# Kernel optimization log

Hardware: AMD Instinct MI355X
Metric: run time of the kernel (lower is better)

Reference implementation:

```python
import jax, jax.numpy as jnp
import numpy as np
import math

N = 50000
E = 1_600_000
F_IN = 512
F_OUT = 256
TAO = 3.0


def setup_inputs() -> dict:
    key = jax.random.key(0)
    ks = jax.random.split(key, 12)
    stdv = 1.0 / math.sqrt(F_OUT)
    std_att = 1.0 / math.sqrt(F_OUT)
    std_att_vec = 1.0 / math.sqrt(3)
    inp = {
        "inputx": jax.random.normal(ks[0], (N, F_IN), dtype=jnp.float32),
        "adj_row": jax.random.randint(ks[1], (E,), 0, N, dtype=jnp.int32),
        "adj_col": jax.random.randint(ks[2], (E,), 0, N, dtype=jnp.int32),
        "adj_val": jax.random.uniform(ks[3], (E,), dtype=jnp.float32),
        "sadj_row": jax.random.randint(ks[4], (E,), 0, N, dtype=jnp.int32),
        "sadj_col": jax.random.randint(ks[5], (E,), 0, N, dtype=jnp.int32),
        "sadj_val": jax.random.uniform(ks[6], (E,), dtype=jnp.float32),
        "weight_mlp": jax.random.uniform(ks[7], (F_IN, F_OUT), minval=-stdv, maxval=stdv, dtype=jnp.float32),
        "weight_A": jax.random.uniform(ks[8], (F_IN, F_OUT), minval=-stdv, maxval=stdv, dtype=jnp.float32),
        "weight_As": jax.random.uniform(ks[9], (F_IN, F_OUT), minval=-stdv, maxval=stdv, dtype=jnp.float32),
        "att_vec_k": jax.random.uniform(ks[10], (F_OUT, F_OUT), minval=-std_att, maxval=std_att, dtype=jnp.float32),
        "att_vec_v": jax.random.uniform(ks[11], (3, 3), minval=-std_att_vec, maxval=std_att_vec, dtype=jnp.float32),
    }
    return inp


def _spmm(row, col, val, h):
    # sparse [N,N] @ dense [N,F]: gather source rows, scale, scatter-add to dest
    msgs = val[:, None] * h[col]  # [E, F]
    return jax.ops.segment_sum(msgs, row, num_segments=N)


def reference(inputx, adj_row, adj_col, adj_val, sadj_row, sadj_col, sadj_val,
              weight_mlp, weight_A, weight_As, att_vec_k, att_vec_v):
    output_mlp = jax.nn.relu(inputx @ weight_mlp)                     # [N, F]
    output_A = jax.nn.relu(_spmm(adj_row, adj_col, adj_val, inputx @ weight_A))
    output_As = jax.nn.relu(_spmm(sadj_row, sadj_col, sadj_val, inputx @ weight_As))

    output_stru = output_mlp + output_As + output_A
    K = jnp.mean(output_stru @ att_vec_k, axis=0, keepdims=True)      # [1, F]
    logits = jnp.concatenate([output_mlp @ K.T, output_A @ K.T, output_As @ K.T], axis=1)  # [N, 3]
    att = jax.nn.softmax((jax.nn.sigmoid(logits) @ att_vec_v) / TAO, axis=1)
    alpha_mlp, alpha_A, alpha_As = att[:, 0:1], att[:, 1:2], att[:, 2:3]
    emb = alpha_mlp * output_mlp + alpha_A * output_A + alpha_As * output_As
    return emb
```

## Files before the change

### kernel.cpp

```cpp
#include <hip/hip_runtime.h>
#include <hip/hip_bf16.h>

#define N_NODES 50000
#define E_EDGES 1600000
#define FIN 512
#define FOUT 256
#define NCOMB 768
#define TAO_F 3.0f
#define M_PAD 50048
#define NB 196
#define CSTRIDE 16
#define CH 4096
#define NCH 13

#define GEMM_WGS 2346
#define GEMM_Q  (GEMM_WGS / 8)
#define GEMM_R  (GEMM_WGS % 8)

typedef __bf16 bf16x8 __attribute__((ext_vector_type(8)));
typedef float  f32x4  __attribute__((ext_vector_type(4)));

static __device__ __forceinline__ unsigned short f2bf(float f) {
    unsigned int u = __float_as_uint(f);
    u += 0x7FFFu + ((u >> 16) & 1u);
    return (unsigned short)(u >> 16);
}
static __device__ __forceinline__ float bf2f(unsigned short h) {
    return __uint_as_float(((unsigned int)h) << 16);
}

__global__ void convert_x_kernel(const float* __restrict__ X, unsigned short* __restrict__ Xb) {
    long long i = ((long long)blockIdx.x * blockDim.x + threadIdx.x) * 4;
    const long long total = (long long)M_PAD * FIN;
    if (i >= total) return;
    const long long valid = (long long)N_NODES * FIN;
    ushort4 o;
    if (i < valid) {
        const float4 v = *reinterpret_cast<const float4*>(X + i);
        o.x = f2bf(v.x); o.y = f2bf(v.y); o.z = f2bf(v.z); o.w = f2bf(v.w);
    } else {
        o.x = o.y = o.z = o.w = 0;
    }
    *reinterpret_cast<ushort4*>(Xb + i) = o;
}

__global__ void convert_w_kernel(const float* __restrict__ Wm, const float* __restrict__ Wa,
                                 const float* __restrict__ Was, unsigned short* __restrict__ Wt) {
    int i = blockIdx.x * blockDim.x + threadIdx.x;
    if (i >= NCOMB * FIN) return;
    int row = i / FIN, k = i % FIN;
    int w = row >> 8, n = row & 255;
    const float* W = (w == 0) ? Wm : (w == 1) ? Wa : Was;
    Wt[i] = f2bf(W[(size_t)k * FOUT + n]);
}

#define BM 128
#define BN 128
#define BK 64

__global__ __launch_bounds__(256) void gemm_kernel(const unsigned short* __restrict__ A,
                                                   const unsigned short* __restrict__ Bt,
                                                   float* __restrict__ Omlp,
                                                   unsigned short* __restrict__ HA,
                                                   unsigned short* __restrict__ HAs) {
    __shared__ unsigned short As[BM * BK];
    __shared__ unsigned short Bs[BN * BK];
    const int b = blockIdx.x;
    const int xcd = b & 7, ii = b >> 3;
    const int work = (xcd < GEMM_R ? xcd * (GEMM_Q + 1)
                                   : GEMM_R * (GEMM_Q + 1) + (xcd - GEMM_R) * GEMM_Q) + ii;
    const int py = work / 6, px = work - py * 6;
    const int row0 = py * BM, col0 = px * BN;
    const int tid = threadIdx.x;
    const int lane = tid & 63, wave = tid >> 6;
    const int wr = wave >> 1, wc = wave & 1;
    const int st_row = tid >> 3;
    const int st_col = (tid & 7) * 8;
    const int lds_off = wave * 512;
    const unsigned short* Ag = A + (size_t)(row0 + st_row) * FIN + st_col;
    const unsigned short* Bg = Bt + (size_t)(col0 + st_row) * FIN + st_col;
    f32x4 acc[4][4] = {};

    for (int k0 = 0; k0 < FIN; k0 += BK) {
#pragma unroll
        for (int i = 0; i < 4; i++) {
            __builtin_amdgcn_global_load_lds(
                (const __attribute__((address_space(1))) unsigned int*)(Ag + (size_t)i * 32 * FIN + k0),
                (__attribute__((address_space(3))) unsigned int*)&As[i * 2048 + lds_off], 16, 0, 0);
            __builtin_amdgcn_global_load_lds(
                (const __attribute__((address_space(1))) unsigned int*)(Bg + (size_t)i * 32 * FIN + k0),
                (__attribute__((address_space(3))) unsigned int*)&Bs[i * 2048 + lds_off], 16, 0, 0);
        }
        __syncthreads();
#pragma unroll
        for (int kk = 0; kk < 2; kk++) {
            bf16x8 af[4], bfr[4];
            const int ko = kk * 32 + (lane >> 4) * 8;
#pragma unroll
            for (int m = 0; m < 4; m++)
                af[m] = *reinterpret_cast<const bf16x8*>(&As[(wr * 64 + m * 16 + (lane & 15)) * BK + ko]);
#pragma unroll
            for (int n = 0; n < 4; n++)
                bfr[n] = *reinterpret_cast<const bf16x8*>(&Bs[(wc * 64 + n * 16 + (lane & 15)) * BK + ko]);
#pragma unroll
            for (int m = 0; m < 4; m++)
#pragma unroll
                for (int n = 0; n < 4; n++)
                    acc[m][n] = __builtin_amdgcn_mfma_f32_16x16x32_bf16(af[m], bfr[n], acc[m][n], 0, 0, 0);
        }
        __syncthreads();
    }

    const int seg = col0 >> 8;
    unsigned short* hp = (seg == 1) ? HA : HAs;
    const int rb = row0 + wr * 64 + ((lane >> 4) << 2);
    const int cb = col0 + wc * 64 + (lane & 15) - seg * 256;
#pragma unroll
    for (int m = 0; m < 4; m++)
#pragma unroll
        for (int n = 0; n < 4; n++)
#pragma unroll
            for (int j = 0; j < 4; j++) {
                int r = rb + m * 16 + j;
                if (r < N_NODES) {
                    float v = acc[m][n][j];
                    int c = cb + n * 16;
                    if (seg == 0) Omlp[(size_t)r * FOUT + c] = fmaxf(v, 0.f);
                    else          hp[(size_t)r * FOUT + c] = f2bf(v);
                }
            }
}

__global__ __launch_bounds__(256) void hist_kernel(const int* __restrict__ rowA, int* __restrict__ bcntA,
                                                   const int* __restrict__ rowS, int* __restrict__ bcntS) {
    __shared__ int h[2 * NB];
    const int t = threadIdx.x;
    for (int j = t; j < 2 * NB; j += 256) h[j] = 0;
    __syncthreads();
    int i = blockIdx.x * blockDim.x + t;
    const int stride = gridDim.x * blockDim.x;
    for (; i < E_EDGES; i += stride) {
        atomicAdd(&h[rowA[i] >> 8], 1);
        atomicAdd(&h[NB + (rowS[i] >> 8)], 1);
    }
    __syncthreads();
    for (int j = t; j < 2 * NB; j += 256) {
        int v = h[j];
        if (v) {
            if (j < NB) atomicAdd(&bcntA[j * CSTRIDE], v);
            else        atomicAdd(&bcntS[(j - NB) * CSTRIDE], v);
        }
    }
}

__global__ __launch_bounds__(256) void scan196_kernel(const int* __restrict__ bcntA, int* __restrict__ bstartA,
                                                      int* __restrict__ bcurA,
                                                      const int* __restrict__ bcntS, int* __restrict__ bstartS,
                                                      int* __restrict__ bcurS) {
    __shared__ int wsum[4];
    const int t = threadIdx.x, lane = t & 63, w = t >> 6;
    for (int g = 0; g < 2; g++) {
        const int* bcnt = g ? bcntS : bcntA;
        int* bstart = g ? bstartS : bstartA;
        int* bcur = g ? bcurS : bcurA;
        int v = (t < NB) ? bcnt[t * CSTRIDE] : 0;
        int x = v;
#pragma unroll
        for (int off = 1; off < 64; off <<= 1) { int y = __shfl_up(x, off); if (lane >= off) x += y; }
        if (lane == 63) wsum[w] = x;
        __syncthreads();
        int woff = 0;
        for (int i = 0; i < w; i++) woff += wsum[i];
        int ex = woff + x - v;
        if (t < NB) { bstart[t] = ex; bcur[t * CSTRIDE] = ex; }
        if (t == 0) bstart[NB] = E_EDGES;
        __syncthreads();
    }
}

__global__ __launch_bounds__(256) void pass1_kernel(
    const int* __restrict__ rowA, const int* __restrict__ colA, const float* __restrict__ valA,
    int* __restrict__ bcurA, int2* __restrict__ ed1A,
    const int* __restrict__ rowS, const int* __restrict__ colS, const float* __restrict__ valS,
    int* __restrict__ bcurS, int2* __restrict__ ed1S) {
    __shared__ int lcnt[NB];
    __shared__ int gcur[NB];
    const int t = threadIdx.x;
    const int base = blockIdx.x * CH;
    const int n = min(CH, E_EDGES - base);
    for (int g = 0; g < 2; g++) {
        const int* row = g ? rowS : rowA;
        const int* col = g ? colS : colA;
        const float* val = g ? valS : valA;
        int* bcur = g ? bcurS : bcurA;
        int2* ed1 = g ? ed1S : ed1A;
        for (int j = t; j < NB; j += 256) lcnt[j] = 0;
        __syncthreads();
        for (int j = t; j < n; j += 256) atomicAdd(&lcnt[row[base + j] >> 8], 1);
        __syncthreads();
        for (int j = t; j < NB; j += 256) {
            int c = lcnt[j];
            gcur[j] = c ? atomicAdd(&bcur[j * CSTRIDE], c) : 0;
        }
        __syncthreads();
        for (int j = t; j < n; j += 256) {
            int r = row[base + j];
            int b = r >> 8;
            int pos = atomicAdd(&gcur[b], 1);
            ed1[pos] = make_int2(((r & 255) << 16) | col[base + j], __float_as_int(val[base + j]));
        }
        __syncthreads();
    }
}

__global__ __launch_bounds__(256) void pass2_kernel(
    const int* __restrict__ bstartA, const int2* __restrict__ ed1A, int2* __restrict__ ed2A, int* __restrict__ rpA,
    const int* __restrict__ bstartS, const int2* __restrict__ ed1S, int2* __restrict__ ed2S, int* __restrict__ rpS) {
    const int g = (blockIdx.x >= NB) ? 1 : 0;
    const int b = blockIdx.x - g * NB;
    const int* bstart = g ? bstartS : bstartA;
    const int2* ed1 = g ? ed1S : ed1A;
    int2* ed2 = g ? ed2S : ed2A;
    int* rp = g ? rpS : rpA;
    const int s = bstart[b], e = bstart[b + 1];
    const int t = threadIdx.x, lane = t & 63, w = t >> 6;
    __shared__ int rcnt[256 * NCH];
    __shared__ int lcur[256 * NCH];
    __shared__ int wsum[4];
    for (int j = t; j < 256 * NCH; j += 256) rcnt[j] = 0;
    __syncthreads();
    for (int j = s + t; j < e; j += 256) {
        int2 v2 = ed1[j];
        atomicAdd(&rcnt[(v2.x >> 16) * NCH + ((v2.x & 0xFFFF) >> 12)], 1);
    }
    __syncthreads();
    int rsum = 0;
#pragma unroll
    for (int c = 0; c < NCH; c++) rsum += rcnt[t * NCH + c];
    int x = rsum;
#pragma unroll
    for (int off = 1; off < 64; off <<= 1) { int y = __shfl_up(x, off); if (lane >= off) x += y; }
    if (lane == 63) wsum[w] = x;
    __syncthreads();
    int woff = 0;
    for (int i = 0; i < w; i++) woff += wsum[i];
    const int ex = woff + x - rsum;
    const int row = b * 256 + t;
    if (row < N_NODES) rp[row] = s + ex;
    if (b == NB - 1 && t == 0) rp[N_NODES] = E_EDGES;
    int off2 = ex;
#pragma unroll
    for (int c = 0; c < NCH; c++) { lcur[t * NCH + c] = off2; off2 += rcnt[t * NCH + c]; }
    __syncthreads();
    for (int j = s + t; j < e; j += 256) {
        int2 v2 = ed1[j];
        int rl = v2.x >> 16, cc = (v2.x & 0xFFFF) >> 12;
        int k = atomicAdd(&lcur[rl * NCH + cc], 1);
        ed2[s + k] = make_int2(v2.x & 0xFFFF, v2.y);
    }
}

__global__ __launch_bounds__(256) void spmm_kernel(
    const int* __restrict__ rpA, const int2* __restrict__ edA,
    const unsigned short* __restrict__ HA, unsigned short* __restrict__ OA,
    const int* __restrict__ rpS, const int2* __restrict__ edS,
    const unsigned short* __restrict__ HS, unsigned short* __restrict__ OS) {
    const int gw = blockIdx.x * 4 + (threadIdx.x >> 6);
    const int lane = threadIdx.x & 63;
    const int* rp; const int2* ed; const unsigned short* H; unsigned short* O; int r;
    if (gw < N_NODES) { rp = rpA; ed = edA; H = HA; O = OA; r = gw; }
    else              { rp = rpS; ed = edS; H = HS; O = OS; r = gw - N_NODES; }
    const int s = rp[r], e = rp[r + 1];
    float a0 = 0.f, a1 = 0.f, a2 = 0.f, a3 = 0.f;
#pragma unroll 4
    for (int i = s; i < e; ++i) {
        const int2 ev = ed[i];
        const float v = __int_as_float(ev.y);
        const uint2 hv = *reinterpret_cast<const uint2*>(H + (((size_t)ev.x) << 8) + lane * 4);
        a0 += v * bf2f((unsigned short)(hv.x & 0xFFFFu));
        a1 += v * bf2f((unsigned short)(hv.x >> 16));
        a2 += v * bf2f((unsigned short)(hv.y & 0xFFFFu));
        a3 += v * bf2f((unsigned short)(hv.y >> 16));
    }
    ushort4 o;
    o.x = f2bf(fmaxf(a0, 0.f));
    o.y = f2bf(fmaxf(a1, 0.f));
    o.z = f2bf(fmaxf(a2, 0.f));
    o.w = f2bf(fmaxf(a3, 0.f));
    *reinterpret_cast<ushort4*>(O + (((size_t)r) << 8) + lane * 4) = o;
}

__global__ void colsum_kernel(const float* __restrict__ Om, const unsigned short* __restrict__ Oa,
                              const unsigned short* __restrict__ Oas, float* __restrict__ colsum) {
    const int t = threadIdx.x;
    float acc = 0.f;
    for (int r = blockIdx.x; r < N_NODES; r += gridDim.x) {
        size_t o = (size_t)r * FOUT + t;
        acc += Om[o] + bf2f(Oa[o]) + bf2f(Oas[o]);
    }
    atomicAdd(&colsum[t], acc);
}

__global__ void kvec_kernel(const float* __restrict__ colsum, const float* __restrict__ attk,
                            float* __restrict__ Kv) {
    __shared__ float mean_s[FOUT];
    const int t = threadIdx.x;
    mean_s[t] = colsum[t] * (1.0f / (float)N_NODES);
    __syncthreads();
    float acc = 0.f;
    for (int i = 0; i < FOUT; i++) acc += mean_s[i] * attk[(size_t)i * FOUT + t];
    Kv[t] = acc;
}

__global__ __launch_bounds__(256) void final_kernel(float* __restrict__ OmOut, const unsigned short* __restrict__ Oa,
                                                    const unsigned short* __restrict__ Oas, const float* __restrict__ Kv,
                                                    const float* __restrict__ attv) {
    const int r = blockIdx.x, t = threadIdx.x, lane = t & 63, w = t >> 6;
    __shared__ float red[4][3];
    __shared__ float alpha[3];
    const size_t o = (size_t)r * FOUT + t;
    const float om = OmOut[o], oa = bf2f(Oa[o]), oas = bf2f(Oas[o]);
    const float kv = Kv[t];
    float p0 = om * kv, p1 = oa * kv, p2 = oas * kv;
#pragma unroll
    for (int off = 32; off; off >>= 1) {
        p0 += __shfl_down(p0, off);
        p1 += __shfl_down(p1, off);
        p2 += __shfl_down(p2, off);
    }
    if (lane == 0) { red[w][0] = p0; red[w][1] = p1; red[w][2] = p2; }
    __syncthreads();
    if (t == 0) {
        float l0 = red[0][0] + red[1][0] + red[2][0] + red[3][0];
        float l1 = red[0][1] + red[1][1] + red[2][1] + red[3][1];
        float l2 = red[0][2] + red[1][2] + red[2][2] + red[3][2];
        float s0 = 1.f / (1.f + __expf(-l0));
        float s1 = 1.f / (1.f + __expf(-l1));
        float s2 = 1.f / (1.f + __expf(-l2));
        float q0 = (s0 * attv[0] + s1 * attv[3] + s2 * attv[6]) * (1.f / TAO_F);
        float q1 = (s0 * attv[1] + s1 * attv[4] + s2 * attv[7]) * (1.f / TAO_F);
        float q2 = (s0 * attv[2] + s1 * attv[5] + s2 * attv[8]) * (1.f / TAO_F);
        float mx = fmaxf(q0, fmaxf(q1, q2));
        float e0 = __expf(q0 - mx), e1 = __expf(q1 - mx), e2 = __expf(q2 - mx);
        float inv = 1.f / (e0 + e1 + e2);
        alpha[0] = e0 * inv; alpha[1] = e1 * inv; alpha[2] = e2 * inv;
    }
    __syncthreads();
    OmOut[o] = alpha[0] * om + alpha[1] * oa + alpha[2] * oas;
}

extern "C" void kernel_launch(void* const* d_in, const int* in_sizes, int n_in,
                              void* d_out, int out_size, void* d_ws, size_t ws_size,
                              hipStream_t stream) {
    (void)in_sizes; (void)n_in; (void)out_size; (void)ws_size;
    const float* X        = (const float*)d_in[0];
    const int*   adj_row  = (const int*)d_in[1];
    const int*   adj_col  = (const int*)d_in[2];
    const float* adj_val  = (const float*)d_in[3];
    const int*   sadj_row = (const int*)d_in[4];
    const int*   sadj_col = (const int*)d_in[5];
    const float* sadj_val = (const float*)d_in[6];
    const float* W_mlp    = (const float*)d_in[7];
    const float* W_A      = (const float*)d_in[8];
    const float* W_As     = (const float*)d_in[9];
    const float* attk     = (const float*)d_in[10];
    const float* attv     = (const float*)d_in[11];
    float* out = (float*)d_out;

    char* p = (char*)d_ws;
    auto alloc = [&](size_t bytes) -> char* {
        char* q = p; p += (bytes + 255) & ~(size_t)255; return q;
    };
    unsigned short* Xb   = (unsigned short*)alloc((size_t)M_PAD * FIN * 2);
    unsigned short* Wt   = (unsigned short*)alloc((size_t)NCOMB * FIN * 2);
    unsigned short* H_A  = (unsigned short*)alloc((size_t)N_NODES * FOUT * 2);
    unsigned short* H_As = (unsigned short*)alloc((size_t)N_NODES * FOUT * 2);
    unsigned short* O_A  = (unsigned short*)alloc((size_t)N_NODES * FOUT * 2);
    unsigned short* O_As = (unsigned short*)alloc((size_t)N_NODES * FOUT * 2);
    int2*  ed1A  = (int2*)alloc((size_t)E_EDGES * 8);
    int2*  ed1S  = (int2*)alloc((size_t)E_EDGES * 8);
    int2*  ed2A  = (int2*)alloc((size_t)E_EDGES * 8);
    int2*  ed2S  = (int2*)alloc((size_t)E_EDGES * 8);
    int*   bcntA = (int*)alloc((size_t)NB * CSTRIDE * 4);
    int*   bcntS = (int*)alloc((size_t)NB * CSTRIDE * 4);
    int*   bcurA = (int*)alloc((size_t)NB * CSTRIDE * 4);
    int*   bcurS = (int*)alloc((size_t)NB * CSTRIDE * 4);
    int*   bstartA = (int*)alloc((size_t)(NB + 1) * 4);
    int*   bstartS = (int*)alloc((size_t)(NB + 1) * 4);
    int*   rpA   = (int*)alloc((size_t)(N_NODES + 1) * 4);
    int*   rpS   = (int*)alloc((size_t)(N_NODES + 1) * 4);
    float* colsum = (float*)alloc(FOUT * 4);
    float* Kv     = (float*)alloc(FOUT * 4);

    hipMemsetAsync(bcntA, 0, (size_t)NB * CSTRIDE * 4, stream);
    hipMemsetAsync(bcntS, 0, (size_t)NB * CSTRIDE * 4, stream);
    hipMemsetAsync(colsum, 0, FOUT * 4, stream);

    {
        long long total = (long long)M_PAD * FIN / 4;
        int blocks = (int)((total + 255) / 256);
        convert_x_kernel<<<blocks, 256, 0, stream>>>(X, Xb);
    }
    convert_w_kernel<<<(NCOMB * FIN + 255) / 256, 256, 0, stream>>>(W_mlp, W_A, W_As, Wt);

    hist_kernel<<<512, 256, 0, stream>>>(adj_row, bcntA, sadj_row, bcntS);
    scan196_kernel<<<1, 256, 0, stream>>>(bcntA, bstartA, bcurA, bcntS, bstartS, bcurS);
    pass1_kernel<<<(E_EDGES + CH - 1) / CH, 256, 0, stream>>>(
        adj_row, adj_col, adj_val, bcurA, ed1A,
        sadj_row, sadj_col, sadj_val, bcurS, ed1S);
    pass2_kernel<<<2 * NB, 256, 0, stream>>>(bstartA, ed1A, ed2A, rpA,
                                             bstartS, ed1S, ed2S, rpS);

    gemm_kernel<<<GEMM_WGS, 256, 0, stream>>>(Xb, Wt, out, H_A, H_As);

    spmm_kernel<<<(2 * N_NODES) / 4, 256, 0, stream>>>(rpA, ed2A, H_A, O_A, rpS, ed2S, H_As, O_As);

    colsum_kernel<<<512, 256, 0, stream>>>(out, O_A, O_As, colsum);
    kvec_kernel<<<1, 256, 0, stream>>>(colsum, attk, Kv);
    final_kernel<<<N_NODES, 256, 0, stream>>>(out, O_A, O_As, Kv, attv);
}
```

Measured before the change: 566.2 us.

## Fuse column-sum into GEMM and SpMM epilogues, store MLP output as bf16

Removes the separate colsum kernel. Column sums are now accumulated in the GEMM epilogue for the MLP branch and in the SpMM kernel for the two graph branches, using LDS atomics followed by global atomics spread over 8 XCD-striped copies. The MLP output is stored as bf16 in a workspace buffer instead of fp32 in the output, which cuts write and read traffic. The SpMM now processes 8 consecutive rows per wave, with padded row pointers so the tail needs no bounds check. Trade-offs are bf16 rounding of the MLP branch, extra atomic traffic, and coarser SpMM load balance.

```diff
diff --git a/kernel.cpp b/kernel.cpp
--- a/kernel.cpp
+++ b/kernel.cpp
@@ -8,10 +8,13 @@
 #define NCOMB 768
 #define TAO_F 3.0f
 #define M_PAD 50048
+#define N_RPAD 50048
 #define NB 196
 #define CSTRIDE 16
 #define CH 4096
 #define NCH 13
+#define RPW 8
+#define WPG 6256
 
 #define GEMM_WGS 2346
 #define GEMM_Q  (GEMM_WGS / 8)
@@ -60,11 +63,13 @@
 
 __global__ __launch_bounds__(256) void gemm_kernel(const unsigned short* __restrict__ A,
                                                    const unsigned short* __restrict__ Bt,
-                                                   float* __restrict__ Omlp,
+                                                   unsigned short* __restrict__ Hm,
                                                    unsigned short* __restrict__ HA,
-                                                   unsigned short* __restrict__ HAs) {
+                                                   unsigned short* __restrict__ HAs,
+                                                   float* __restrict__ colsum8) {
     __shared__ unsigned short As[BM * BK];
     __shared__ unsigned short Bs[BN * BK];
+    __shared__ float csm[128];
     const int b = blockIdx.x;
     const int xcd = b & 7, ii = b >> 3;
     const int work = (xcd < GEMM_R ? xcd * (GEMM_Q + 1)
@@ -74,6 +79,7 @@
     const int tid = threadIdx.x;
     const int lane = tid & 63, wave = tid >> 6;
     const int wr = wave >> 1, wc = wave & 1;
+    if (tid < 128) csm[tid] = 0.f;
     const int st_row = tid >> 3;
     const int st_col = (tid & 7) * 8;
     const int lds_off = wave * 512;
@@ -112,9 +118,11 @@
     }
 
     const int seg = col0 >> 8;
-    unsigned short* hp = (seg == 1) ? HA : HAs;
+    unsigned short* hp = (seg == 0) ? Hm : (seg == 1) ? HA : HAs;
     const int rb = row0 + wr * 64 + ((lane >> 4) << 2);
-    const int cb = col0 + wc * 64 + (lane & 15) - seg * 256;
+    const int cb_loc = wc * 64 + (lane & 15);
+    const int cbase = col0 - seg * 256 + cb_loc;
+    float part[4] = {0.f, 0.f, 0.f, 0.f};
 #pragma unroll
     for (int m = 0; m < 4; m++)
 #pragma unroll
@@ -124,11 +132,16 @@
                 int r = rb + m * 16 + j;
                 if (r < N_NODES) {
                     float v = acc[m][n][j];
-                    int c = cb + n * 16;
-                    if (seg == 0) Omlp[(size_t)r * FOUT + c] = fmaxf(v, 0.f);
-                    else          hp[(size_t)r * FOUT + c] = f2bf(v);
+                    if (seg == 0) { v = fmaxf(v, 0.f); part[n] += v; }
+                    hp[(size_t)r * FOUT + cbase + n * 16] = f2bf(v);
                 }
             }
+    if (seg == 0) {
+#pragma unroll
+        for (int n = 0; n < 4; n++) atomicAdd(&csm[cb_loc + n * 16], part[n]);
+        __syncthreads();
+        if (tid < 128) atomicAdd(&colsum8[((b & 7) << 8) + col0 + tid], csm[tid]);
+    }
 }
 
 __global__ __launch_bounds__(256) void hist_kernel(const int* __restrict__ rowA, int* __restrict__ bcntA,
@@ -247,7 +260,7 @@
     const int ex = woff + x - rsum;
     const int row = b * 256 + t;
     if (row < N_NODES) rp[row] = s + ex;
-    if (b == NB - 1 && t == 0) rp[N_NODES] = E_EDGES;
+    else if (row <= N_RPAD) rp[row] = E_EDGES;
     int off2 = ex;
 #pragma unroll
     for (int c = 0; c < NCH; c++) { lcur[t * NCH + c] = off2; off2 += rcnt[t * NCH + c]; }
@@ -264,62 +277,80 @@
     const int* __restrict__ rpA, const int2* __restrict__ edA,
     const unsigned short* __restrict__ HA, unsigned short* __restrict__ OA,
     const int* __restrict__ rpS, const int2* __restrict__ edS,
-    const unsigned short* __restrict__ HS, unsigned short* __restrict__ OS) {
-    const int gw = blockIdx.x * 4 + (threadIdx.x >> 6);
-    const int lane = threadIdx.x & 63;
-    const int* rp; const int2* ed; const unsigned short* H; unsigned short* O; int r;
-    if (gw < N_NODES) { rp = rpA; ed = edA; H = HA; O = OA; r = gw; }
-    else              { rp = rpS; ed = edS; H = HS; O = OS; r = gw - N_NODES; }
-    const int s = rp[r], e = rp[r + 1];
-    float a0 = 0.f, a1 = 0.f, a2 = 0.f, a3 = 0.f;
+    const unsigned short* __restrict__ HS, unsigned short* __restrict__ OS,
+    float* __restrict__ colsum8) {
+    __shared__ float csum[256];
+    const int t = threadIdx.x, wave = t >> 6, lane = t & 63;
+    csum[t] = 0.f;
+    __syncthreads();
+    const int gwave = blockIdx.x * 4 + wave;
+    const int g = (gwave >= WPG) ? 1 : 0;
+    const int wv = gwave - g * WPG;
+    const int* rp = g ? rpS : rpA;
+    const int2* ed = g ? edS : edA;
+    const unsigned short* H = g ? HS : HA;
+    unsigned short* O = g ? OS : OA;
+    const int r0 = wv * RPW;
+    float cs0 = 0.f, cs1 = 0.f, cs2 = 0.f, cs3 = 0.f;
+    int s = rp[r0];
+#pragma unroll
+    for (int i = 0; i < RPW; i++) {
+        const int r = r0 + i;
+        const int e = rp[r + 1];
+        float a0 = 0.f, a1 = 0.f, a2 = 0.f, a3 = 0.f;
 #pragma unroll 4
-    for (int i = s; i < e; ++i) {
-        const int2 ev = ed[i];
-        const float v = __int_as_float(ev.y);
-        const uint2 hv = *reinterpret_cast<const uint2*>(H + (((size_t)ev.x) << 8) + lane * 4);
-        a0 += v * bf2f((unsigned short)(hv.x & 0xFFFFu));
-        a1 += v * bf2f((unsigned short)(hv.x >> 16));
-        a2 += v * bf2f((unsigned short)(hv.y & 0xFFFFu));
-        a3 += v * bf2f((unsigned short)(hv.y >> 16));
-    }
-    ushort4 o;
-    o.x = f2bf(fmaxf(a0, 0.f));
-    o.y = f2bf(fmaxf(a1, 0.f));
-    o.z = f2bf(fmaxf(a2, 0.f));
-    o.w = f2bf(fmaxf(a3, 0.f));
-    *reinterpret_cast<ushort4*>(O + (((size_t)r) << 8) + lane * 4) = o;
-}
-
-__global__ void colsum_kernel(const float* __restrict__ Om, const unsigned short* __restrict__ Oa,
-                              const unsigned short* __restrict__ Oas, float* __restrict__ colsum) {
-    const int t = threadIdx.x;
-    float acc = 0.f;
-    for (int r = blockIdx.x; r < N_NODES; r += gridDim.x) {
-        size_t o = (size_t)r * FOUT + t;
-        acc += Om[o] + bf2f(Oa[o]) + bf2f(Oas[o]);
-    }
-    atomicAdd(&colsum[t], acc);
-}
-
-__global__ void kvec_kernel(const float* __restrict__ colsum, const float* __restrict__ attk,
+        for (int j = s; j < e; ++j) {
+            const int2 ev = ed[j];
+            const float v = __int_as_float(ev.y);
+            const uint2 hv = *reinterpret_cast<const uint2*>(H + (((size_t)ev.x) << 8) + lane * 4);
+            a0 += v * bf2f((unsigned short)(hv.x & 0xFFFFu));
+            a1 += v * bf2f((unsigned short)(hv.x >> 16));
+            a2 += v * bf2f((unsigned short)(hv.y & 0xFFFFu));
+            a3 += v * bf2f((unsigned short)(hv.y >> 16));
+        }
+        s = e;
+        if (r < N_NODES) {
+            a0 = fmaxf(a0, 0.f); a1 = fmaxf(a1, 0.f);
+            a2 = fmaxf(a2, 0.f); a3 = fmaxf(a3, 0.f);
+            cs0 += a0; cs1 += a1; cs2 += a2; cs3 += a3;
+            ushort4 o;
+            o.x = f2bf(a0); o.y = f2bf(a1); o.z = f2bf(a2); o.w = f2bf(a3);
+            *reinterpret_cast<ushort4*>(O + (((size_t)r) << 8) + lane * 4) = o;
+        }
+    }
+    atomicAdd(&csum[lane * 4 + 0], cs0);
+    atomicAdd(&csum[lane * 4 + 1], cs1);
+    atomicAdd(&csum[lane * 4 + 2], cs2);
+    atomicAdd(&csum[lane * 4 + 3], cs3);
+    __syncthreads();
+    atomicAdd(&colsum8[((blockIdx.x & 7) << 8) + t], csum[t]);
+}
+
+__global__ void kvec_kernel(const float* __restrict__ colsum8, const float* __restrict__ attk,
                             float* __restrict__ Kv) {
     __shared__ float mean_s[FOUT];
     const int t = threadIdx.x;
-    mean_s[t] = colsum[t] * (1.0f / (float)N_NODES);
+    float cs = 0.f;
+#pragma unroll
+    for (int k = 0; k < 8; k++) cs += colsum8[(k << 8) + t];
+    mean_s[t] = cs * (1.0f / (float)N_NODES);
     __syncthreads();
     float acc = 0.f;
     for (int i = 0; i < FOUT; i++) acc += mean_s[i] * attk[(size_t)i * FOUT + t];
     Kv[t] = acc;
 }
 
-__global__ __launch_bounds__(256) void final_kernel(float* __restrict__ OmOut, const unsigned short* __restrict__ Oa,
-                                                    const unsigned short* __restrict__ Oas, const float* __restrict__ Kv,
+__global__ __launch_bounds__(256) void final_kernel(float* __restrict__ out,
+                                                    const unsigned short* __restrict__ Omb,
+                                                    const unsigned short* __restrict__ Oa,
+                                                    const unsigned short* __restrict__ Oas,
+                                                    const float* __restrict__ Kv,
                                                     const float* __restrict__ attv) {
     const int r = blockIdx.x, t = threadIdx.x, lane = t & 63, w = t >> 6;
     __shared__ float red[4][3];
     __shared__ float alpha[3];
     const size_t o = (size_t)r * FOUT + t;
-    const float om = OmOut[o], oa = bf2f(Oa[o]), oas = bf2f(Oas[o]);
+    const float om = bf2f(Omb[o]), oa = bf2f(Oa[o]), oas = bf2f(Oas[o]);
     const float kv = Kv[t];
     float p0 = om * kv, p1 = oa * kv, p2 = oas * kv;
 #pragma unroll
@@ -346,7 +377,7 @@
         alpha[0] = e0 * inv; alpha[1] = e1 * inv; alpha[2] = e2 * inv;
     }
     __syncthreads();
-    OmOut[o] = alpha[0] * om + alpha[1] * oa + alpha[2] * oas;
+    out[o] = alpha[0] * om + alpha[1] * oa + alpha[2] * oas;
 }
 
 extern "C" void kernel_launch(void* const* d_in, const int* in_sizes, int n_in,
@@ -373,6 +404,7 @@
     };
     unsigned short* Xb   = (unsigned short*)alloc((size_t)M_PAD * FIN * 2);
     unsigned short* Wt   = (unsigned short*)alloc((size_t)NCOMB * FIN * 2);
+    unsigned short* H_M  = (unsigned short*)alloc((size_t)N_NODES * FOUT * 2);
     unsigned short* H_A  = (unsigned short*)alloc((size_t)N_NODES * FOUT * 2);
     unsigned short* H_As = (unsigned short*)alloc((size_t)N_NODES * FOUT * 2);
     unsigned short* O_A  = (unsigned short*)alloc((size_t)N_NODES * FOUT * 2);
@@ -387,14 +419,14 @@
     int*   bcurS = (int*)alloc((size_t)NB * CSTRIDE * 4);
     int*   bstartA = (int*)alloc((size_t)(NB + 1) * 4);
     int*   bstartS = (int*)alloc((size_t)(NB + 1) * 4);
-    int*   rpA   = (int*)alloc((size_t)(N_NODES + 1) * 4);
-    int*   rpS   = (int*)alloc((size_t)(N_NODES + 1) * 4);
-    float* colsum = (float*)alloc(FOUT * 4);
-    float* Kv     = (float*)alloc(FOUT * 4);
+    int*   rpA   = (int*)alloc((size_t)(N_RPAD + 1) * 4);
+    int*   rpS   = (int*)alloc((size_t)(N_RPAD + 1) * 4);
+    float* colsum8 = (float*)alloc(8 * FOUT * 4);
+    float* Kv      = (float*)alloc(FOUT * 4);
 
     hipMemsetAsync(bcntA, 0, (size_t)NB * CSTRIDE * 4, stream);
     hipMemsetAsync(bcntS, 0, (size_t)NB * CSTRIDE * 4, stream);
-    hipMemsetAsync(colsum, 0, FOUT * 4, stream);
+    hipMemsetAsync(colsum8, 0, 8 * FOUT * 4, stream);
 
     {
         long long total = (long long)M_PAD * FIN / 4;
@@ -411,11 +443,11 @@
     pass2_kernel<<<2 * NB, 256, 0, stream>>>(bstartA, ed1A, ed2A, rpA,
                                              bstartS, ed1S, ed2S, rpS);
 
-    gemm_kernel<<<GEMM_WGS, 256, 0, stream>>>(Xb, Wt, out, H_A, H_As);
-
-    spmm_kernel<<<(2 * N_NODES) / 4, 256, 0, stream>>>(rpA, ed2A, H_A, O_A, rpS, ed2S, H_As, O_As);
-
-    colsum_kernel<<<512, 256, 0, stream>>>(out, O_A, O_As, colsum);
-    kvec_kernel<<<1, 256, 0, stream>>>(colsum, attk, Kv);
-    final_kernel<<<N_NODES, 256, 0, stream>>>(out, O_A, O_As, Kv, attv);
-}
+    gemm_kernel<<<GEMM_WGS, 256, 0, stream>>>(Xb, Wt, H_M, H_A, H_As, colsum8);
+
+    spmm_kernel<<<(2 * WPG) / 4, 256, 0, stream>>>(rpA, ed2A, H_A, O_A,
+                                                   rpS, ed2S, H_As, O_As, colsum8);
+
+    kvec_kernel<<<1, 256, 0, stream>>>(colsum8, attk, Kv);
+    final_kernel<<<N_NODES, 256, 0, stream>>>(out, H_M, O_A, O_As, Kv, attv);
+}
```

Result: faster. 538.8 us (-4.8%).
